# Kernel tuning notes

Hardware: AMD Instinct MI355X
Metric: run time of the kernel (lower is better)

## Reference

```python
import math
import jax, jax.numpy as jnp
import numpy as np

B, IMG, CIN = 32, 32, 4
PATCH, HIDDEN, DEPTH, HEADS, MLP = 2, 768, 12, 12, 3072
FREQ, NUM_CLASSES = 256, 1000
GRID = IMG // PATCH
N = GRID * GRID
OUT = PATCH * PATCH * CIN


def _pos_embed(dim, length):
    # faithful port of get_2d_sincos_pos_embed
    g = int(math.sqrt(length))
    grid = np.stack(np.meshgrid(np.arange(g, dtype=np.float32),
                                np.arange(g, dtype=np.float32), indexing='ij')).reshape(2, -1)
    def emb1d(d, pos):
        omega = 1.0 / 10000.0 ** (np.arange(d // 2, dtype=np.float32) / (d / 2.0))
        out = np.einsum('m,d->md', pos, omega)
        return np.concatenate([np.sin(out), np.cos(out)], axis=1)
    pe = np.concatenate([emb1d(dim // 2, grid[0]), emb1d(dim // 2, grid[1])], axis=1)
    return jnp.asarray(pe[None], dtype=jnp.float32)  # [1, N, dim]


def _ln(x):
    # LayerNorm(elementwise_affine=False), eps=1e-5, biased variance
    m = jnp.mean(x, axis=-1, keepdims=True)
    v = jnp.var(x, axis=-1, keepdims=True)
    return (x - m) * jax.lax.rsqrt(v + 1e-5)


def setup_inputs() -> dict:
    key = jax.random.key(0)
    ks = jax.random.split(key, 20)
    w = lambda k, shape: jax.random.normal(k, shape, jnp.float32) * 0.02
    z = lambda *shape: jnp.zeros(shape, jnp.float32)
    return {
        'x': jax.random.normal(ks[0], (B, IMG, IMG, CIN), jnp.float32),
        't': jax.random.uniform(ks[1], (B,), jnp.float32) * 1000.0,
        'y': jax.random.randint(ks[2], (B,), 0, NUM_CLASSES + 1),
        'patch_w': w(ks[3], (PATCH * PATCH * CIN, HIDDEN)), 'patch_b': z(HIDDEN),
        't_w1': w(ks[4], (FREQ, HIDDEN)), 't_b1': z(HIDDEN),
        't_w2': w(ks[5], (HIDDEN, HIDDEN)), 't_b2': z(HIDDEN),
        'label_emb': w(ks[6], (NUM_CLASSES + 1, HIDDEN)),
        'ada_w': w(ks[7], (DEPTH, HIDDEN, 6 * HIDDEN)), 'ada_b': z(DEPTH, 6 * HIDDEN),
        'q_w': w(ks[8], (DEPTH, HIDDEN, HIDDEN)), 'q_b': z(DEPTH, HIDDEN),
        'k_w': w(ks[9], (DEPTH, HIDDEN, HIDDEN)), 'k_b': z(DEPTH, HIDDEN),
        'v_w': w(ks[10], (DEPTH, HIDDEN, HIDDEN)), 'v_b': z(DEPTH, HIDDEN),
        'o_w': w(ks[11], (DEPTH, HIDDEN, HIDDEN)), 'o_b': z(DEPTH, HIDDEN),
        'fc1_w': w(ks[12], (DEPTH, HIDDEN, MLP)), 'fc1_b': z(DEPTH, MLP),
        'fc2_w': w(ks[13], (DEPTH, MLP, HIDDEN)), 'fc2_b': z(DEPTH, HIDDEN),
        'fin_ada_w': w(ks[14], (HIDDEN, 2 * HIDDEN)), 'fin_ada_b': z(2 * HIDDEN),
        'fin_w': w(ks[15], (HIDDEN, OUT)), 'fin_b': z(OUT),
    }


def reference(x, t, y, patch_w, patch_b, t_w1, t_b1, t_w2, t_b2, label_emb,
              ada_w, ada_b, q_w, q_b, k_w, k_b, v_w, v_b, o_w, o_b,
              fc1_w, fc1_b, fc2_w, fc2_b, fin_ada_w, fin_ada_b, fin_w, fin_b):
    Bx = x.shape[0]
    dh = HIDDEN // HEADS
    # patch embed (conv k=p, stride=p == per-patch linear)
    patches = x.reshape(Bx, GRID, PATCH, GRID, PATCH, CIN)
    patches = patches.transpose(0, 1, 3, 2, 4, 5).reshape(Bx, N, PATCH * PATCH * CIN)
    h = patches @ patch_w + patch_b + _pos_embed(HIDDEN, N)
    # timestep embedding: [cos, sin] order
    half = FREQ // 2
    freqs = jnp.exp(-math.log(10000.0) * jnp.arange(half, dtype=jnp.float32) / half)
    args = t.astype(jnp.float32)[:, None] * freqs[None]
    temb = jnp.concatenate([jnp.cos(args), jnp.sin(args)], axis=-1)
    temb = jax.nn.silu(temb @ t_w1 + t_b1) @ t_w2 + t_b2
    c_act = jax.nn.silu(temb + label_emb[y])  # silu applied inside each block on c

    def block(hx, p):
        aw, ab, qw, qb, kw, kb, vw, vb, ow, ob, f1w, f1b, f2w, f2b = p
        ada = c_act @ aw + ab
        sh_m, sc_m, g_m, sh_p, sc_p, g_p = jnp.split(ada, 6, axis=-1)
        xn = _ln(hx) * (1.0 + sc_m[:, None]) + sh_m[:, None]
        q = ((xn @ qw + qb).reshape(Bx, N, HEADS, dh)) / math.sqrt(3.0)
        k = (xn @ kw + kb).reshape(Bx, N, HEADS, dh)
        v = (xn @ vw + vb).reshape(Bx, N, HEADS, dh)
        attn = jax.nn.softmax(jnp.einsum('bqhc,bkhc->bhqk', q, k).astype(jnp.float32), axis=-1)
        yv = jnp.einsum('bhqk,bkhc->bqhc', attn, v).reshape(Bx, N, HIDDEN)
        hx = hx + g_m[:, None] * (yv @ ow + ob)
        xn2 = _ln(hx) * (1.0 + sc_p[:, None]) + sh_p[:, None]
        mlp = jax.nn.gelu(xn2 @ f1w + f1b, approximate=False) @ f2w + f2b
        hx = hx + g_p[:, None] * mlp
        return hx, None

    h, _ = jax.lax.scan(block, h, (ada_w, ada_b, q_w, q_b, k_w, k_b, v_w, v_b,
                                   o_w, o_b, fc1_w, fc1_b, fc2_w, fc2_b))
    # final layer
    fada = c_act @ fin_ada_w + fin_ada_b
    sh, sc = jnp.split(fada, 2, axis=-1)
    out = (_ln(h) * (1.0 + sc[:, None]) + sh[:, None]) @ fin_w + fin_b
    return out  # [B, N, patch*patch*out_channels]
```

## Files before the change

### kernel.cpp

```cpp
#include <hip/hip_runtime.h>
#include <hip/hip_bf16.h>


typedef short  s16x8 __attribute__((ext_vector_type(8)));
typedef float  f32x4 __attribute__((ext_vector_type(4)));

__device__ __forceinline__ float bf2f(unsigned short u) {
    union { unsigned int i; float f; } v; v.i = ((unsigned int)u) << 16; return v.f;
}
__device__ __forceinline__ unsigned short f2bf(float f) {
    union { float f; unsigned int i; } v; v.f = f;
    unsigned int r = (v.i + 0x7FFFu + ((v.i >> 16) & 1u)) >> 16;
    return (unsigned short)r;
}
__device__ __forceinline__ float silu(float v) { return v / (1.f + __expf(-v)); }

__device__ __forceinline__ void gload16(const void* gptr, void* lptr) {
    __builtin_amdgcn_global_load_lds(
        (const __attribute__((address_space(1))) unsigned int*)gptr,
        (__attribute__((address_space(3))) unsigned int*)lptr,
        16, 0, 0);
}

#define ROWS 8192
#define HID  768
#define MLPD 3072
#define ADA_LD 4608

__global__ __launch_bounds__(256) void ada_init(const float* __restrict__ ada_b,
                                                const float* __restrict__ fada_b,
                                                const float* __restrict__ t_b1,
                                                const float* __restrict__ t_b2,
                                                const float* __restrict__ lemb,
                                                const int* __restrict__ y,
                                                float* __restrict__ ada_all,
                                                float* __restrict__ fada,
                                                float* __restrict__ z1,
                                                float* __restrict__ z2)
{
    const int bid = blockIdx.x, tid = threadIdx.x;
    if (bid >= 222) {
        const int col = (bid - 222) * 256 + tid;
        const float b1v = t_b1[col], b2v = t_b2[col];
        for (int r = 0; r < 32; ++r) {
            z1[(size_t)r * HID + col] = b1v;
            z2[(size_t)r * HID + col] = b2v + lemb[(size_t)y[r] * HID + col];
        }
        return;
    }
    const float* Bv; float* Out; int ldw, colb;
    if (bid < 216) {
        const int l = bid / 18; colb = (bid % 18) * 256;
        Bv = ada_b + (size_t)l * ADA_LD; Out = ada_all + (size_t)l * 32 * ADA_LD; ldw = ADA_LD;
    } else {
        colb = (bid - 216) * 256;
        Bv = fada_b; Out = fada; ldw = 1536;
    }
    const int col = colb + tid;
    const float bb = Bv[col];
    #pragma unroll
    for (int r = 0; r < 32; ++r) Out[(size_t)r * ldw + col] = bb;
}

__global__ __launch_bounds__(256) void temb1_k(const float* __restrict__ t,
                                               const float* __restrict__ w1,
                                               float* __restrict__ z1)
{
    __shared__ float tin[128];
    const int b = blockIdx.x, cc = blockIdx.y, kc = blockIdx.z, tid = threadIdx.x;
    const int k0 = kc * 128;
    if (tid < 128) {
        const int k = k0 + tid, j = k & 127;
        const float fr = __expf((float)j * (-9.210340371976184f / 128.f));
        const float a = t[b] * fr;
        tin[tid] = (k < 128) ? cosf(a) : sinf(a);
    }
    __syncthreads();
    const int col = cc * 256 + tid;
    float acc = 0.f;
    #pragma unroll 8
    for (int kk = 0; kk < 128; ++kk) acc += tin[kk] * w1[(size_t)(k0 + kk) * HID + col];
    atomicAdd(&z1[(size_t)b * HID + col], acc);
}

__global__ __launch_bounds__(256) void temb2_k(const float* __restrict__ z1,
                                               const float* __restrict__ w2,
                                               float* __restrict__ z2)
{
    __shared__ float tin[192];
    const int b = blockIdx.x, cc = blockIdx.y, kc = blockIdx.z, tid = threadIdx.x;
    const int k0 = kc * 192;
    if (tid < 192) tin[tid] = silu(z1[(size_t)b * HID + k0 + tid]);
    __syncthreads();
    const int col = cc * 256 + tid;
    float acc = 0.f;
    #pragma unroll 8
    for (int kk = 0; kk < 192; ++kk) acc += tin[kk] * w2[(size_t)(k0 + kk) * HID + col];
    atomicAdd(&z2[(size_t)b * HID + col], acc);
}

__global__ __launch_bounds__(256) void csilu_k(const float* __restrict__ z2,
                                               unsigned short* __restrict__ cact_bf)
{
    const int base = (blockIdx.x * 256 + threadIdx.x) * 8;
    #pragma unroll
    for (int i = 0; i < 8; ++i)
        cact_bf[base + i] = f2bf(silu(z2[base + i]));
}

__global__ __launch_bounds__(256) void ada_gemm2(const float* __restrict__ z2,
                                                 const float* __restrict__ ada_w,
                                                 const float* __restrict__ fada_w,
                                                 float* __restrict__ ada_all,
                                                 float* __restrict__ fada)
{
    const int bx = blockIdx.x, kc = blockIdx.y, tid = threadIdx.x;
    const float* W; float* Out; int ldw, colb;
    if (bx < 216) {
        const int l = bx / 18; colb = (bx % 18) * 256;
        W = ada_w + (size_t)l * HID * ADA_LD; Out = ada_all + (size_t)l * 32 * ADA_LD; ldw = ADA_LD;
    } else {
        colb = (bx - 216) * 256;
        W = fada_w; Out = fada; ldw = 1536;
    }
    const int col = colb + tid;
    const int k0 = kc * 96;
    __shared__ float cs_[32][96];
    for (int i = tid; i < 32 * 96; i += 256)
        cs_[i / 96][i % 96] = silu(z2[(size_t)(i / 96) * HID + k0 + (i % 96)]);
    __syncthreads();
    float acc[32];
    #pragma unroll
    for (int r = 0; r < 32; ++r) acc[r] = 0.f;
    #pragma unroll 2
    for (int kk = 0; kk < 96; kk += 4) {
        const float w0 = W[(size_t)(k0 + kk) * ldw + col];
        const float w1 = W[(size_t)(k0 + kk + 1) * ldw + col];
        const float w2 = W[(size_t)(k0 + kk + 2) * ldw + col];
        const float w3 = W[(size_t)(k0 + kk + 3) * ldw + col];
        #pragma unroll
        for (int r = 0; r < 32; ++r) {
            const float4 cv = *(const float4*)&cs_[r][kk];
            acc[r] += cv.x * w0 + cv.y * w1 + cv.z * w2 + cv.w * w3;
        }
    }
    #pragma unroll
    for (int r = 0; r < 32; ++r) atomicAdd(&Out[(size_t)r * ldw + col], acc[r]);
}

__global__ __launch_bounds__(256) void ada_mfma(const unsigned short* __restrict__ cact_bf,
                                                const unsigned short* __restrict__ adaT,
                                                const unsigned short* __restrict__ fadaT,
                                                const float* __restrict__ ada_b,
                                                const float* __restrict__ fada_b,
                                                float* __restrict__ ada_all,
                                                float* __restrict__ fada)
{
    __shared__ unsigned short sB[2][8192];
    const int bx = blockIdx.x, tid = threadIdx.x;
    const unsigned short* Bt; const float* bias; float* Out; int ldw, colb;
    if (bx < 216) {
        const int l = bx / 18; colb = (bx % 18) * 256;
        Bt = adaT + (size_t)l * ADA_LD * HID;
        bias = ada_b + (size_t)l * ADA_LD;
        Out = ada_all + (size_t)l * 32 * ADA_LD; ldw = ADA_LD;
    } else {
        colb = (bx - 216) * 256;
        Bt = fadaT; bias = fada_b; Out = fada; ldw = 1536;
    }
    const int lane = tid & 63, w = tid >> 6;
    const int lm = lane & 15, lg = lane >> 4;
    auto stageB = [&](int buf, int kt) {
        #pragma unroll
        for (int g = 0; g < 4; ++g) {
            const int gi = g * 256 + tid;
            const int col = gi >> 2, k8 = (gi & 3) * 8;
            gload16(Bt + (size_t)(colb + col) * HID + kt * 32 + k8,
                    &sB[buf][0] + (size_t)gi * 8);
        }
    };
    f32x4 acc[2][4];
    #pragma unroll
    for (int i = 0; i < 2; ++i)
        #pragma unroll
        for (int j = 0; j < 4; ++j) acc[i][j] = (f32x4){0.f, 0.f, 0.f, 0.f};
    stageB(0, 0);
    __syncthreads();
    int cur = 0;
    for (int kt = 0; kt < 24; ++kt) {
        if (kt + 1 < 24) stageB(cur ^ 1, kt + 1);
        s16x8 af[2], bfr[4];
        #pragma unroll
        for (int mi = 0; mi < 2; ++mi)
            af[mi] = *(const s16x8*)(cact_bf + (size_t)(mi * 16 + lm) * HID + kt * 32 + lg * 8);
        #pragma unroll
        for (int nj = 0; nj < 4; ++nj)
            bfr[nj] = *(const s16x8*)&sB[cur][(w * 64 + nj * 16 + lm) * 32 + lg * 8];
        #pragma unroll
        for (int mi = 0; mi < 2; ++mi)
            #pragma unroll
            for (int nj = 0; nj < 4; ++nj)
                acc[mi][nj] = __builtin_amdgcn_mfma_f32_16x16x32_bf16(af[mi], bfr[nj], acc[mi][nj], 0, 0, 0);
        __syncthreads();
        cur ^= 1;
    }
    #pragma unroll
    for (int mi = 0; mi < 2; ++mi) {
        const int row = mi * 16 + (lg << 2);
        #pragma unroll
        for (int nj = 0; nj < 4; ++nj) {
            const int col = colb + w * 64 + nj * 16 + lm;
            const float bb = bias[col];
            #pragma unroll
            for (int r = 0; r < 4; ++r)
                Out[(size_t)(row + r) * ldw + col] = acc[mi][nj][r] + bb;
        }
    }
}

__global__ __launch_bounds__(256) void patch_embed(const float* __restrict__ x,
                                                   const float* __restrict__ pw,
                                                   const float* __restrict__ pb,
                                                   float* __restrict__ h)
{
    const int row = blockIdx.x;
    const int b = row >> 8, n = row & 255;
    const int gi = n >> 4, gj = n & 15;
    const int tid = threadIdx.x;
    __shared__ float pv[16];
    if (tid < 16) {
        const int pr = tid >> 3, pc = (tid >> 2) & 1, ci = tid & 3;
        pv[tid] = x[((size_t)(b * 32 + gi * 2 + pr) * 32 + (gj * 2 + pc)) * 4 + ci];
    }
    __syncthreads();
    #pragma unroll
    for (int cc = 0; cc < 3; ++cc) {
        const int col = cc * 256 + tid;
        float acc = pb[col];
        #pragma unroll
        for (int i = 0; i < 16; ++i) acc += pv[i] * pw[(size_t)i * HID + col];
        const int d4 = (col < 384) ? col : col - 384;
        const int pos = (col < 384) ? gi : gj;
        const float kf = (float)(d4 < 192 ? d4 : d4 - 192);
        const float om = __expf(kf * (-9.210340371976184f / 192.f));
        const float a = (float)pos * om;
        acc += (d4 < 192) ? sinf(a) : cosf(a);
        h[(size_t)row * HID + col] = acc;
    }
}

__global__ __launch_bounds__(256) void convert_weights(
    const float* __restrict__ q_w, const float* __restrict__ k_w,
    const float* __restrict__ v_w, const float* __restrict__ o_w,
    const float* __restrict__ fc1_w, const float* __restrict__ fc2_w,
    const float* __restrict__ q_b, const float* __restrict__ k_b,
    const float* __restrict__ v_b,
    unsigned short* __restrict__ wbase, size_t slot_stride,
    float* __restrict__ cbias, int first_layer)
{
    const int bid = blockIdx.x;
    const int l = first_layer + bid / 6913;
    const int t = bid % 6913;
    unsigned short* dst = wbase + (size_t)(bid / 6913) * slot_stride;
    const int tid = threadIdx.x;
    if (t == 6912) {
        float* cb = cbias + (size_t)l * 2304;
        for (int i = tid; i < 2304; i += 256) {
            float v;
            if (i < 768)       v = q_b[(size_t)l * 768 + i];
            else if (i < 1536) v = k_b[(size_t)l * 768 + i - 768];
            else               v = v_b[(size_t)l * 768 + i - 1536];
            cb[i] = v;
        }
        return;
    }
    const float* src; int srcN; unsigned short* d; int dLd; int tr, tc;
    if (t < 2304) {
        const int mat = t / 576, tt = t % 576; tr = tt / 24; tc = tt % 24;
        srcN = 768; dLd = 768;
        if (mat == 0)      { src = q_w + (size_t)l * 589824; d = dst; }
        else if (mat == 1) { src = k_w + (size_t)l * 589824; d = dst + 589824; }
        else if (mat == 2) { src = v_w + (size_t)l * 589824; d = dst + 1179648; }
        else               { src = o_w + (size_t)l * 589824; d = dst + 1769472; }
    } else if (t < 4608) {
        const int tt = t - 2304; tr = tt / 96; tc = tt % 96;
        src = fc1_w + (size_t)l * 2359296; srcN = 3072; dLd = 768; d = dst + 2359296;
    } else {
        const int tt = t - 4608; tr = tt / 24; tc = tt % 24;
        src = fc2_w + (size_t)l * 2359296; srcN = 768; dLd = 3072; d = dst + 4718592;
    }
    __shared__ float lt[32][33];
    const int tx = tid & 31, ty = tid >> 5;
    const int r0 = tr * 32, c0 = tc * 32;
    #pragma unroll
    for (int i = 0; i < 4; ++i)
        lt[ty + i * 8][tx] = src[(size_t)(r0 + ty + i * 8) * srcN + c0 + tx];
    __syncthreads();
    const int q = tid & 15;
    const int cw = tid >> 4;
    #pragma unroll
    for (int i = 0; i < 2; ++i) {
        const int cc = cw + i * 16;
        const unsigned int pk = (unsigned int)f2bf(lt[2 * q][cc])
                              | ((unsigned int)f2bf(lt[2 * q + 1][cc]) << 16);
        *(unsigned int*)&d[(size_t)(c0 + cc) * dLd + r0 + 2 * q] = pk;
    }
}

__global__ __launch_bounds__(256) void convert_ada(
    const float* __restrict__ ada_w, const float* __restrict__ fada_w,
    unsigned short* __restrict__ adaT, unsigned short* __restrict__ fadaT)
{
    const int bid = blockIdx.x, tid = threadIdx.x;
    const float* src; unsigned short* d; int srcN, tr, tc;
    if (bid < 41472) {
        const int l = bid / 3456, tt = bid % 3456;
        tr = tt / 144; tc = tt % 144;
        src = ada_w + (size_t)l * HID * ADA_LD; srcN = ADA_LD;
        d = adaT + (size_t)l * ADA_LD * HID;
    } else {
        const int tt = bid - 41472;
        tr = tt / 48; tc = tt % 48;
        src = fada_w; srcN = 1536; d = fadaT;
    }
    __shared__ float lt[32][33];
    const int tx = tid & 31, ty = tid >> 5;
    const int r0 = tr * 32, c0 = tc * 32;
    #pragma unroll
    for (int i = 0; i < 4; ++i)
        lt[ty + i * 8][tx] = src[(size_t)(r0 + ty + i * 8) * srcN + c0 + tx];
    __syncthreads();
    const int q = tid & 15;
    const int cw = tid >> 4;
    #pragma unroll
    for (int i = 0; i < 2; ++i) {
        const int cc = cw + i * 16;
        const unsigned int pk = (unsigned int)f2bf(lt[2 * q][cc])
                              | ((unsigned int)f2bf(lt[2 * q + 1][cc]) << 16);
        *(unsigned int*)&d[(size_t)(c0 + cc) * HID + r0 + 2 * q] = pk;
    }
}

__global__ __launch_bounds__(192) void ln_mod(const float* __restrict__ hbuf,
                                              const float* __restrict__ mod,
                                              int sh_off, int sc_off, int mld,
                                              unsigned short* __restrict__ xout)
{
    const int row = blockIdx.x, tid = threadIdx.x;
    const float4 xv = *(const float4*)&hbuf[(size_t)row * HID + tid * 4];
    float s = (xv.x + xv.y) + (xv.z + xv.w);
    float ss = (xv.x * xv.x + xv.y * xv.y) + (xv.z * xv.z + xv.w * xv.w);
    #pragma unroll
    for (int d = 1; d < 64; d <<= 1) { s += __shfl_xor(s, d); ss += __shfl_xor(ss, d); }
    __shared__ float sb[3], ssb[3];
    if ((tid & 63) == 0) { sb[tid >> 6] = s; ssb[tid >> 6] = ss; }
    __syncthreads();
    s = sb[0] + sb[1] + sb[2];
    ss = ssb[0] + ssb[1] + ssb[2];
    const float mean = s * (1.f / 768.f);
    const float var = ss * (1.f / 768.f) - mean * mean;
    const float rs = rsqrtf(var + 1e-5f);
    const int b = row >> 8;
    const float* mrow = mod + (size_t)b * mld;
    const float4 sc = *(const float4*)&mrow[sc_off + tid * 4];
    const float4 sh = *(const float4*)&mrow[sh_off + tid * 4];
    ushort4 o;
    o.x = f2bf((xv.x - mean) * rs * (1.f + sc.x) + sh.x);
    o.y = f2bf((xv.y - mean) * rs * (1.f + sc.y) + sh.y);
    o.z = f2bf((xv.z - mean) * rs * (1.f + sc.z) + sh.z);
    o.w = f2bf((xv.w - mean) * rs * (1.f + sc.w) + sh.w);
    *(ushort4*)&xout[(size_t)row * HID + tid * 4] = o;
}

template<int EPI, int BN>
__global__ __launch_bounds__(256) void gemm_bt(const unsigned short* __restrict__ A,
                                               const unsigned short* __restrict__ Bt,
                                               const float* __restrict__ bias,
                                               void* __restrict__ outp,
                                               const float* __restrict__ gate,
                                               int K, int ldo)
{
    constexpr int BELEMS = BN * 32;
    constexpr int NJ = BN / 32;
    __shared__ unsigned short sAB[2][4096 + BELEMS];
    const int tid = threadIdx.x;
    const int lane = tid & 63;
    const int w = tid >> 6;
    const int wm = w >> 1, wn = w & 1;
    const int nwg = gridDim.x * gridDim.y;
    int bidl = blockIdx.y * gridDim.x + blockIdx.x;
    bidl = (bidl & 7) * (nwg >> 3) + (bidl >> 3);
    const int bx = bidl % gridDim.x, by = bidl / gridDim.x;
    const int rowbase = by << 7;
    const int colbase = bx * BN;
    const size_t a0 = (size_t)(rowbase +      (tid >> 2)) * K + (tid & 3) * 8;
    const size_t a1 = (size_t)(rowbase + 64 + (tid >> 2)) * K + (tid & 3) * 8;
    const size_t b0 = (size_t)(colbase +      (tid >> 2)) * K + (tid & 3) * 8;
    size_t b1 = 0;
    if constexpr (BN == 128)
        b1 = (size_t)(colbase + 64 + (tid >> 2)) * K + (tid & 3) * 8;
    const int ldsw = w * 512;
    f32x4 acc[4][NJ];
    #pragma unroll
    for (int i = 0; i < 4; ++i)
        #pragma unroll
        for (int j = 0; j < NJ; ++j) acc[i][j] = (f32x4){0.f, 0.f, 0.f, 0.f};
    const int nk = K >> 5;
    const int lm = lane & 15, lg = lane >> 4;
    {
        unsigned short* base = &sAB[0][0];
        gload16(A + a0,  base + ldsw);
        gload16(A + a1,  base + 2048 + ldsw);
        gload16(Bt + b0, base + 4096 + ldsw);
        if constexpr (BN == 128) gload16(Bt + b1, base + 6144 + ldsw);
    }
    __syncthreads();
    int cur = 0;
    for (int kt = 0; kt < nk; ++kt) {
        if (kt + 1 < nk) {
            const int k0 = (kt + 1) << 5;
            unsigned short* base = &sAB[cur ^ 1][0];
            gload16(A + a0 + k0,  base + ldsw);
            gload16(A + a1 + k0,  base + 2048 + ldsw);
            gload16(Bt + b0 + k0, base + 4096 + ldsw);
            if constexpr (BN == 128) gload16(Bt + b1 + k0, base + 6144 + ldsw);
        }
        const unsigned short* sAc = &sAB[cur][0];
        const unsigned short* sBc = &sAB[cur][4096];
        s16x8 af[4], bfr[NJ];
        #pragma unroll
        for (int mi = 0; mi < 4; ++mi)
            af[mi] = *(const s16x8*)&sAc[(wm * 64 + mi * 16 + lm) * 32 + lg * 8];
        #pragma unroll
        for (int nj = 0; nj < NJ; ++nj)
            bfr[nj] = *(const s16x8*)&sBc[(wn * (16 * NJ) + nj * 16 + lm) * 32 + lg * 8];
        #pragma unroll
        for (int mi = 0; mi < 4; ++mi)
            #pragma unroll
            for (int nj = 0; nj < NJ; ++nj)
                acc[mi][nj] = __builtin_amdgcn_mfma_f32_16x16x32_bf16(af[mi], bfr[nj], acc[mi][nj], 0, 0, 0);
        __syncthreads();
        cur ^= 1;
    }
    float bv[NJ], gv[NJ];
    #pragma unroll
    for (int nj = 0; nj < NJ; ++nj) {
        const int col = colbase + wn * (16 * NJ) + nj * 16 + lm;
        bv[nj] = bias[col];
        if constexpr (EPI == 2) gv[nj] = gate[(size_t)(rowbase >> 8) * ADA_LD + col];
    }
    #pragma unroll
    for (int mi = 0; mi < 4; ++mi) {
        const int row = rowbase + wm * 64 + mi * 16 + (lg << 2);
        #pragma unroll
        for (int nj = 0; nj < NJ; ++nj) {
            const int col = colbase + wn * (16 * NJ) + nj * 16 + lm;
            #pragma unroll
            for (int r = 0; r < 4; ++r) {
                const float v = acc[mi][nj][r] + bv[nj];
                if constexpr (EPI == 0) {
                    ((unsigned short*)outp)[(size_t)(row + r) * ldo + col] = f2bf(v);
                } else if constexpr (EPI == 1) {
                    const float g = 0.5f * v * (1.f + erff(v * 0.70710678118654752f));
                    ((unsigned short*)outp)[(size_t)(row + r) * ldo + col] = f2bf(g);
                } else {
                    float* O = (float*)outp;
                    const size_t idx = (size_t)(row + r) * ldo + col;
                    O[idx] = O[idx] + gv[nj] * v;
                }
            }
        }
    }
}

__global__ __launch_bounds__(256) void attn_fused(const unsigned short* __restrict__ qkv,
                                                  unsigned short* __restrict__ yv)
{
    __shared__ unsigned short Vt[64][264];
    __shared__ unsigned short Psm[4][32 * 72];
    __shared__ float Ssc[4][32];
    const int bid = blockIdx.x;
    const int b = bid / 24, rem = bid % 24, h = rem >> 1, half = rem & 1;
    const int tid = threadIdx.x, w = tid >> 6, lane = tid & 63;
    {
        const int dhg = tid & 7, tk = tid >> 3;
        #pragma unroll
        for (int g = 0; g < 8; ++g) {
            const int tok = tk + g * 32;
            s16x8 vv = *(const s16x8*)(qkv + (size_t)(b * 256 + tok) * 2304 + 1536 + h * 64 + dhg * 8);
            #pragma unroll
            for (int j = 0; j < 8; ++j) Vt[dhg * 8 + j][tok] = (unsigned short)vv[j];
        }
    }
    __syncthreads();
    const int q0 = half * 128 + w * 32;
    const int lm = lane & 15, lg = lane >> 4;
    const unsigned short* Qb = qkv + (size_t)(b * 256 + q0) * 2304 + h * 64;
    s16x8 qf[2][2];
    #pragma unroll
    for (int ni = 0; ni < 2; ++ni)
        #pragma unroll
        for (int kk = 0; kk < 2; ++kk)
            qf[ni][kk] = *(const s16x8*)(Qb + (size_t)(ni * 16 + lm) * 2304 + kk * 32 + lg * 8);
    f32x4 o_[2][4];
    #pragma unroll
    for (int i = 0; i < 2; ++i)
        #pragma unroll
        for (int j = 0; j < 4; ++j) o_[i][j] = (f32x4){0.f, 0.f, 0.f, 0.f};
    float m_[2], l_[2];
    #pragma unroll
    for (int i = 0; i < 2; ++i) { m_[i] = -1e30f; l_[i] = 0.f; }
    const float s3 = 0.57735026918962576f;
    for (int c = 0; c < 4; ++c) {
        f32x4 st[4][2];
        #pragma unroll
        for (int i = 0; i < 4; ++i)
            #pragma unroll
            for (int j = 0; j < 2; ++j) st[i][j] = (f32x4){0.f, 0.f, 0.f, 0.f};
        const unsigned short* Kb = qkv + (size_t)(b * 256 + c * 64) * 2304 + 768 + h * 64;
        __builtin_amdgcn_s_setprio(1);
        #pragma unroll
        for (int kk = 0; kk < 2; ++kk)
            #pragma unroll
            for (int mi = 0; mi < 4; ++mi) {
                const s16x8 kf = *(const s16x8*)(Kb + (size_t)(mi * 16 + lm) * 2304 + kk * 32 + lg * 8);
                #pragma unroll
                for (int ni = 0; ni < 2; ++ni)
                    st[mi][ni] = __builtin_amdgcn_mfma_f32_16x16x32_bf16(kf, qf[ni][kk], st[mi][ni], 0, 0, 0);
            }
        __builtin_amdgcn_s_setprio(0);
        #pragma unroll
        for (int ni = 0; ni < 2; ++ni) {
            float cm = -1e30f;
            #pragma unroll
            for (int mi = 0; mi < 4; ++mi)
                #pragma unroll
                for (int r = 0; r < 4; ++r) cm = fmaxf(cm, st[mi][ni][r]);
            cm = fmaxf(cm, __shfl_xor(cm, 16));
            cm = fmaxf(cm, __shfl_xor(cm, 32));
            cm *= s3;
            const float mn = fmaxf(m_[ni], cm);
            const float corr = __expf(m_[ni] - mn);
            float cs = 0.f;
            #pragma unroll
            for (int mi = 0; mi < 4; ++mi) {
                float p0 = __expf(st[mi][ni][0] * s3 - mn);
                float p1 = __expf(st[mi][ni][1] * s3 - mn);
                float p2 = __expf(st[mi][ni][2] * s3 - mn);
                float p3 = __expf(st[mi][ni][3] * s3 - mn);
                cs += (p0 + p1) + (p2 + p3);
                uint2 pk;
                pk.x = (unsigned int)f2bf(p0) | ((unsigned int)f2bf(p1) << 16);
                pk.y = (unsigned int)f2bf(p2) | ((unsigned int)f2bf(p3) << 16);
                *(uint2*)&Psm[w][(ni * 16 + lm) * 72 + mi * 16 + lg * 4] = pk;
            }
            cs += __shfl_xor(cs, 16);
            cs += __shfl_xor(cs, 32);
            l_[ni] = l_[ni] * corr + cs;
            m_[ni] = mn;
            if (lane < 16) Ssc[w][ni * 16 + lane] = corr;
        }
        asm volatile("" ::: "memory");
        #pragma unroll
        for (int qi = 0; qi < 2; ++qi) {
            float fr[4];
            #pragma unroll
            for (int r = 0; r < 4; ++r) fr[r] = Ssc[w][qi * 16 + lg * 4 + r];
            #pragma unroll
            for (int di = 0; di < 4; ++di)
                #pragma unroll
                for (int r = 0; r < 4; ++r) o_[qi][di][r] *= fr[r];
        }
        __builtin_amdgcn_s_setprio(1);
        #pragma unroll
        for (int kk = 0; kk < 2; ++kk)
            #pragma unroll
            for (int qi = 0; qi < 2; ++qi) {
                const s16x8 pa = *(const s16x8*)&Psm[w][(qi * 16 + lm) * 72 + kk * 32 + lg * 8];
                #pragma unroll
                for (int di = 0; di < 4; ++di) {
                    const s16x8 vb = *(const s16x8*)&Vt[di * 16 + lm][c * 64 + kk * 32 + lg * 8];
                    o_[qi][di] = __builtin_amdgcn_mfma_f32_16x16x32_bf16(pa, vb, o_[qi][di], 0, 0, 0);
                }
            }
        __builtin_amdgcn_s_setprio(0);
    }
    asm volatile("" ::: "memory");
    if (lane < 16) {
        #pragma unroll
        for (int ni = 0; ni < 2; ++ni) Ssc[w][ni * 16 + lane] = 1.f / l_[ni];
    }
    asm volatile("" ::: "memory");
    #pragma unroll
    for (int qi = 0; qi < 2; ++qi) {
        float fr[4];
        #pragma unroll
        for (int r = 0; r < 4; ++r) fr[r] = Ssc[w][qi * 16 + lg * 4 + r];
        #pragma unroll
        for (int di = 0; di < 4; ++di)
            #pragma unroll
            for (int r = 0; r < 4; ++r) {
                const float val = o_[qi][di][r] * fr[r];
                yv[(size_t)(b * 256 + q0 + qi * 16 + lg * 4 + r) * HID + h * 64 + di * 16 + lm] = f2bf(val);
            }
    }
}

__global__ __launch_bounds__(256) void fin_gemm(const unsigned short* __restrict__ xn,
                                                const float* __restrict__ w,
                                                const float* __restrict__ bias,
                                                float* __restrict__ out)
{
    __shared__ unsigned short xs[16 * 768];
    const int rb = blockIdx.x * 16, tid = threadIdx.x;
    #pragma unroll
    for (int i = 0; i < 6; ++i) {
        const int v = tid + i * 256;
        const int row = v / 96, koff = (v % 96) * 8;
        *(s16x8*)&xs[v * 8] = *(const s16x8*)(xn + (size_t)(rb + row) * HID + koff);
    }
    __syncthreads();
    const int r = tid >> 4, o = tid & 15;
    float acc = bias[o];
    #pragma unroll 8
    for (int k = 0; k < 768; ++k) acc += bf2f(xs[r * 768 + k]) * w[(size_t)k * 16 + o];
    out[(size_t)(rb + r) * 16 + o] = acc;
}

extern "C" void kernel_launch(void* const* d_in, const int* in_sizes, int n_in,
                              void* d_out, int out_size, void* d_ws, size_t ws_size,
                              hipStream_t stream)
{
    const float* x        = (const float*)d_in[0];
    const float* t        = (const float*)d_in[1];
    const int*   y        = (const int*)d_in[2];
    const float* patch_w  = (const float*)d_in[3];
    const float* patch_b  = (const float*)d_in[4];
    const float* t_w1     = (const float*)d_in[5];
    const float* t_b1     = (const float*)d_in[6];
    const float* t_w2     = (const float*)d_in[7];
    const float* t_b2     = (const float*)d_in[8];
    const float* label_e  = (const float*)d_in[9];
    const float* ada_w    = (const float*)d_in[10];
    const float* ada_b    = (const float*)d_in[11];
    const float* q_w      = (const float*)d_in[12];
    const float* q_b      = (const float*)d_in[13];
    const float* k_w      = (const float*)d_in[14];
    const float* k_b      = (const float*)d_in[15];
    const float* v_w      = (const float*)d_in[16];
    const float* v_b      = (const float*)d_in[17];
    const float* o_w      = (const float*)d_in[18];
    const float* o_b      = (const float*)d_in[19];
    const float* fc1_w    = (const float*)d_in[20];
    const float* fc1_b    = (const float*)d_in[21];
    const float* fc2_w    = (const float*)d_in[22];
    const float* fc2_b    = (const float*)d_in[23];
    const float* fada_w   = (const float*)d_in[24];
    const float* fada_b   = (const float*)d_in[25];
    const float* fin_w    = (const float*)d_in[26];
    const float* fin_b    = (const float*)d_in[27];

    char* ws = (char*)d_ws;
    size_t off = 0;
    auto alloc = [&](size_t bytes) { size_t o = off; off = (off + bytes + 255) & ~(size_t)255; return o; };
    const size_t OFF_H     = alloc((size_t)ROWS * HID * 4);
    const size_t OFF_XN    = alloc((size_t)ROWS * HID * 2);
    const size_t OFF_QKV   = alloc((size_t)ROWS * 2304 * 2);
    const size_t OFF_YV    = alloc((size_t)ROWS * HID * 2);
    const size_t OFF_MLP   = alloc((size_t)ROWS * MLPD * 2);
    const size_t OFF_ADA   = alloc((size_t)12 * 32 * ADA_LD * 4);
    const size_t OFF_FADA  = alloc((size_t)32 * 1536 * 4);
    const size_t OFF_Z2    = alloc((size_t)32 * HID * 4);
    const size_t OFF_Z1    = alloc((size_t)32 * HID * 4);
    const size_t OFF_CB    = alloc((size_t)12 * 2304 * 4);
    const size_t OFF_CBF   = alloc((size_t)32 * HID * 2);
    const size_t OFF_ADAT  = alloc((size_t)12 * ADA_LD * HID * 2);
    const size_t OFF_FADAT = alloc((size_t)1536 * HID * 2);
    const size_t OFF_W     = off;
    const size_t WSLOT_ELEMS = 7077888;
    const bool big = (ws_size >= OFF_W + (size_t)12 * WSLOT_ELEMS * 2);

    float*          h     = (float*)(ws + OFF_H);
    unsigned short* xn    = (unsigned short*)(ws + OFF_XN);
    unsigned short* qkv   = (unsigned short*)(ws + OFF_QKV);
    unsigned short* yv    = (unsigned short*)(ws + OFF_YV);
    unsigned short* mlp   = (unsigned short*)(ws + OFF_MLP);
    float*          adaA  = (float*)(ws + OFF_ADA);
    float*          fada  = (float*)(ws + OFF_FADA);
    float*          z2    = (float*)(ws + OFF_Z2);
    float*          z1    = (float*)(ws + OFF_Z1);
    float*          cbias = (float*)(ws + OFF_CB);
    unsigned short* cactb = (unsigned short*)(ws + OFF_CBF);
    unsigned short* adaT  = (unsigned short*)(ws + OFF_ADAT);
    unsigned short* fadaT = (unsigned short*)(ws + OFF_FADAT);
    unsigned short* wsW   = (unsigned short*)(ws + OFF_W);

    ada_init<<<225, 256, 0, stream>>>(ada_b, fada_b, t_b1, t_b2, label_e, y,
                                      adaA, fada, z1, z2);
    temb1_k<<<dim3(32, 3, 2), 256, 0, stream>>>(t, t_w1, z1);
    temb2_k<<<dim3(32, 3, 4), 256, 0, stream>>>(z1, t_w2, z2);
    if (big) {
        convert_ada<<<42624, 256, 0, stream>>>(ada_w, fada_w, adaT, fadaT);
        csilu_k<<<12, 256, 0, stream>>>(z2, cactb);
        ada_mfma<<<222, 256, 0, stream>>>(cactb, adaT, fadaT, ada_b, fada_b, adaA, fada);
        convert_weights<<<6913 * 12, 256, 0, stream>>>(q_w, k_w, v_w, o_w, fc1_w, fc2_w,
                                                       q_b, k_b, v_b, wsW, WSLOT_ELEMS, cbias, 0);
    } else {
        ada_gemm2<<<dim3(222, 8), 256, 0, stream>>>(z2, ada_w, fada_w, adaA, fada);
    }
    patch_embed<<<8192, 256, 0, stream>>>(x, patch_w, patch_b, h);

    for (int l = 0; l < 12; ++l) {
        unsigned short* wslot = wsW + (big ? (size_t)l * WSLOT_ELEMS : 0);
        if (!big) {
            convert_weights<<<6913, 256, 0, stream>>>(q_w, k_w, v_w, o_w, fc1_w, fc2_w,
                                                      q_b, k_b, v_b, wslot, 0, cbias, l);
        }
        unsigned short* qkvT = wslot;
        unsigned short* oT   = wslot + 1769472;
        unsigned short* f1T  = wslot + 2359296;
        unsigned short* f2T  = wslot + 4718592;
        float* ada_l  = adaA + (size_t)l * 32 * ADA_LD;
        float* cb_l   = cbias + (size_t)l * 2304;

        ln_mod<<<8192, 192, 0, stream>>>(h, ada_l, 0, 768, ADA_LD, xn);
        gemm_bt<0, 128><<<dim3(18, 64), 256, 0, stream>>>(xn, qkvT, cb_l, qkv, nullptr, 768, 2304);
        attn_fused<<<768, 256, 0, stream>>>(qkv, yv);
        gemm_bt<2, 64><<<dim3(12, 64), 256, 0, stream>>>(yv, oT, o_b + (size_t)l * 768, h,
                                                         ada_l + 1536, 768, 768);
        ln_mod<<<8192, 192, 0, stream>>>(h, ada_l, 2304, 3072, ADA_LD, xn);
        gemm_bt<1, 128><<<dim3(24, 64), 256, 0, stream>>>(xn, f1T, fc1_b + (size_t)l * 3072, mlp,
                                                          nullptr, 768, 3072);
        gemm_bt<2, 64><<<dim3(12, 64), 256, 0, stream>>>(mlp, f2T, fc2_b + (size_t)l * 768, h,
                                                         ada_l + 3840, 3072, 768);
    }

    ln_mod<<<8192, 192, 0, stream>>>(h, fada, 0, 768, 1536, xn);
    fin_gemm<<<512, 256, 0, stream>>>(xn, fin_w, fin_b, (float*)d_out);
}
```

Before: 3.404 ms.

## Fuse ada weight transpose-convert into ada GEMM and batch LN rows

Removes the separate convert_ada pass, which transposed and converted all adaLN weights to bf16 through a workspace buffer. ada_mfma now reads the fp32 weights directly and converts and packs them into shared memory while staging. The ada_init launch is trimmed to the three timestep blocks when the MFMA path runs. ln_mod now handles four rows per block with a quarter of the launches, adding extra block barriers, and the inline staging loses the asynchronous global-to-LDS loads.

```diff
diff --git a/kernel.cpp b/kernel.cpp
--- a/kernel.cpp
+++ b/kernel.cpp
@@ -36,9 +36,10 @@
                                                 float* __restrict__ ada_all,
                                                 float* __restrict__ fada,
                                                 float* __restrict__ z1,
-                                                float* __restrict__ z2)
-{
-    const int bid = blockIdx.x, tid = threadIdx.x;
+                                                float* __restrict__ z2,
+                                                int bid0)
+{
+    const int bid = blockIdx.x + bid0, tid = threadIdx.x;
     if (bid >= 222) {
         const int col = (bid - 222) * 256 + tid;
         const float b1v = t_b1[col], b2v = t_b2[col];
@@ -149,8 +150,8 @@
 }
 
 __global__ __launch_bounds__(256) void ada_mfma(const unsigned short* __restrict__ cact_bf,
-                                                const unsigned short* __restrict__ adaT,
-                                                const unsigned short* __restrict__ fadaT,
+                                                const float* __restrict__ ada_w,
+                                                const float* __restrict__ fada_w,
                                                 const float* __restrict__ ada_b,
                                                 const float* __restrict__ fada_b,
                                                 float* __restrict__ ada_all,
@@ -158,25 +159,35 @@
 {
     __shared__ unsigned short sB[2][8192];
     const int bx = blockIdx.x, tid = threadIdx.x;
-    const unsigned short* Bt; const float* bias; float* Out; int ldw, colb;
+    const float* W; const float* bias; float* Out; int ldw, colb;
     if (bx < 216) {
         const int l = bx / 18; colb = (bx % 18) * 256;
-        Bt = adaT + (size_t)l * ADA_LD * HID;
+        W = ada_w + (size_t)l * HID * ADA_LD;
         bias = ada_b + (size_t)l * ADA_LD;
         Out = ada_all + (size_t)l * 32 * ADA_LD; ldw = ADA_LD;
     } else {
         colb = (bx - 216) * 256;
-        Bt = fadaT; bias = fada_b; Out = fada; ldw = 1536;
+        W = fada_w; bias = fada_b; Out = fada; ldw = 1536;
     }
     const int lane = tid & 63, w = tid >> 6;
     const int lm = lane & 15, lg = lane >> 4;
+    const int kp = tid & 15, cg = tid >> 4;
     auto stageB = [&](int buf, int kt) {
-        #pragma unroll
-        for (int g = 0; g < 4; ++g) {
-            const int gi = g * 256 + tid;
-            const int col = gi >> 2, k8 = (gi & 3) * 8;
-            gload16(Bt + (size_t)(colb + col) * HID + kt * 32 + k8,
-                    &sB[buf][0] + (size_t)gi * 8);
+        const float* r0 = W + (size_t)(kt * 32 + 2 * kp) * ldw + colb + cg * 16;
+        const float* r1 = r0 + ldw;
+        unsigned int* dst = (unsigned int*)&sB[buf][0];
+        #pragma unroll
+        for (int c4 = 0; c4 < 4; ++c4) {
+            const float4 a = *(const float4*)(r0 + c4 * 4);
+            const float4 b = *(const float4*)(r1 + c4 * 4);
+            const float av[4] = {a.x, a.y, a.z, a.w};
+            const float bv4[4] = {b.x, b.y, b.z, b.w};
+            #pragma unroll
+            for (int c = 0; c < 4; ++c) {
+                const int col = cg * 16 + c4 * 4 + c;
+                dst[col * 16 + kp] = (unsigned int)f2bf(av[c])
+                                   | ((unsigned int)f2bf(bv4[c]) << 16);
+            }
         }
     };
     f32x4 acc[2][4];
@@ -307,69 +318,40 @@
     }
 }
 
-__global__ __launch_bounds__(256) void convert_ada(
-    const float* __restrict__ ada_w, const float* __restrict__ fada_w,
-    unsigned short* __restrict__ adaT, unsigned short* __restrict__ fadaT)
-{
-    const int bid = blockIdx.x, tid = threadIdx.x;
-    const float* src; unsigned short* d; int srcN, tr, tc;
-    if (bid < 41472) {
-        const int l = bid / 3456, tt = bid % 3456;
-        tr = tt / 144; tc = tt % 144;
-        src = ada_w + (size_t)l * HID * ADA_LD; srcN = ADA_LD;
-        d = adaT + (size_t)l * ADA_LD * HID;
-    } else {
-        const int tt = bid - 41472;
-        tr = tt / 48; tc = tt % 48;
-        src = fada_w; srcN = 1536; d = fadaT;
-    }
-    __shared__ float lt[32][33];
-    const int tx = tid & 31, ty = tid >> 5;
-    const int r0 = tr * 32, c0 = tc * 32;
-    #pragma unroll
-    for (int i = 0; i < 4; ++i)
-        lt[ty + i * 8][tx] = src[(size_t)(r0 + ty + i * 8) * srcN + c0 + tx];
-    __syncthreads();
-    const int q = tid & 15;
-    const int cw = tid >> 4;
-    #pragma unroll
-    for (int i = 0; i < 2; ++i) {
-        const int cc = cw + i * 16;
-        const unsigned int pk = (unsigned int)f2bf(lt[2 * q][cc])
-                              | ((unsigned int)f2bf(lt[2 * q + 1][cc]) << 16);
-        *(unsigned int*)&d[(size_t)(c0 + cc) * HID + r0 + 2 * q] = pk;
-    }
-}
-
 __global__ __launch_bounds__(192) void ln_mod(const float* __restrict__ hbuf,
                                               const float* __restrict__ mod,
                                               int sh_off, int sc_off, int mld,
                                               unsigned short* __restrict__ xout)
 {
-    const int row = blockIdx.x, tid = threadIdx.x;
-    const float4 xv = *(const float4*)&hbuf[(size_t)row * HID + tid * 4];
-    float s = (xv.x + xv.y) + (xv.z + xv.w);
-    float ss = (xv.x * xv.x + xv.y * xv.y) + (xv.z * xv.z + xv.w * xv.w);
-    #pragma unroll
-    for (int d = 1; d < 64; d <<= 1) { s += __shfl_xor(s, d); ss += __shfl_xor(ss, d); }
+    const int tid = threadIdx.x;
     __shared__ float sb[3], ssb[3];
-    if ((tid & 63) == 0) { sb[tid >> 6] = s; ssb[tid >> 6] = ss; }
-    __syncthreads();
-    s = sb[0] + sb[1] + sb[2];
-    ss = ssb[0] + ssb[1] + ssb[2];
-    const float mean = s * (1.f / 768.f);
-    const float var = ss * (1.f / 768.f) - mean * mean;
-    const float rs = rsqrtf(var + 1e-5f);
-    const int b = row >> 8;
-    const float* mrow = mod + (size_t)b * mld;
-    const float4 sc = *(const float4*)&mrow[sc_off + tid * 4];
-    const float4 sh = *(const float4*)&mrow[sh_off + tid * 4];
-    ushort4 o;
-    o.x = f2bf((xv.x - mean) * rs * (1.f + sc.x) + sh.x);
-    o.y = f2bf((xv.y - mean) * rs * (1.f + sc.y) + sh.y);
-    o.z = f2bf((xv.z - mean) * rs * (1.f + sc.z) + sh.z);
-    o.w = f2bf((xv.w - mean) * rs * (1.f + sc.w) + sh.w);
-    *(ushort4*)&xout[(size_t)row * HID + tid * 4] = o;
+    #pragma unroll
+    for (int rr = 0; rr < 4; ++rr) {
+        const int row = blockIdx.x * 4 + rr;
+        const float4 xv = *(const float4*)&hbuf[(size_t)row * HID + tid * 4];
+        float s = (xv.x + xv.y) + (xv.z + xv.w);
+        float ss = (xv.x * xv.x + xv.y * xv.y) + (xv.z * xv.z + xv.w * xv.w);
+        #pragma unroll
+        for (int d = 1; d < 64; d <<= 1) { s += __shfl_xor(s, d); ss += __shfl_xor(ss, d); }
+        if ((tid & 63) == 0) { sb[tid >> 6] = s; ssb[tid >> 6] = ss; }
+        __syncthreads();
+        s = sb[0] + sb[1] + sb[2];
+        ss = ssb[0] + ssb[1] + ssb[2];
+        const float mean = s * (1.f / 768.f);
+        const float var = ss * (1.f / 768.f) - mean * mean;
+        const float rs = rsqrtf(var + 1e-5f);
+        const int b = row >> 8;
+        const float* mrow = mod + (size_t)b * mld;
+        const float4 sc = *(const float4*)&mrow[sc_off + tid * 4];
+        const float4 sh = *(const float4*)&mrow[sh_off + tid * 4];
+        ushort4 o;
+        o.x = f2bf((xv.x - mean) * rs * (1.f + sc.x) + sh.x);
+        o.y = f2bf((xv.y - mean) * rs * (1.f + sc.y) + sh.y);
+        o.z = f2bf((xv.z - mean) * rs * (1.f + sc.z) + sh.z);
+        o.w = f2bf((xv.w - mean) * rs * (1.f + sc.w) + sh.w);
+        *(ushort4*)&xout[(size_t)row * HID + tid * 4] = o;
+        __syncthreads();
+    }
 }
 
 template<int EPI, int BN>
@@ -674,8 +656,6 @@
     const size_t OFF_Z1    = alloc((size_t)32 * HID * 4);
     const size_t OFF_CB    = alloc((size_t)12 * 2304 * 4);
     const size_t OFF_CBF   = alloc((size_t)32 * HID * 2);
-    const size_t OFF_ADAT  = alloc((size_t)12 * ADA_LD * HID * 2);
-    const size_t OFF_FADAT = alloc((size_t)1536 * HID * 2);
     const size_t OFF_W     = off;
     const size_t WSLOT_ELEMS = 7077888;
     const bool big = (ws_size >= OFF_W + (size_t)12 * WSLOT_ELEMS * 2);
@@ -691,18 +671,20 @@
     float*          z1    = (float*)(ws + OFF_Z1);
     float*          cbias = (float*)(ws + OFF_CB);
     unsigned short* cactb = (unsigned short*)(ws + OFF_CBF);
-    unsigned short* adaT  = (unsigned short*)(ws + OFF_ADAT);
-    unsigned short* fadaT = (unsigned short*)(ws + OFF_FADAT);
     unsigned short* wsW   = (unsigned short*)(ws + OFF_W);
 
-    ada_init<<<225, 256, 0, stream>>>(ada_b, fada_b, t_b1, t_b2, label_e, y,
-                                      adaA, fada, z1, z2);
+    if (big) {
+        ada_init<<<3, 256, 0, stream>>>(ada_b, fada_b, t_b1, t_b2, label_e, y,
+                                        adaA, fada, z1, z2, 222);
+    } else {
+        ada_init<<<225, 256, 0, stream>>>(ada_b, fada_b, t_b1, t_b2, label_e, y,
+                                          adaA, fada, z1, z2, 0);
+    }
     temb1_k<<<dim3(32, 3, 2), 256, 0, stream>>>(t, t_w1, z1);
     temb2_k<<<dim3(32, 3, 4), 256, 0, stream>>>(z1, t_w2, z2);
     if (big) {
-        convert_ada<<<42624, 256, 0, stream>>>(ada_w, fada_w, adaT, fadaT);
         csilu_k<<<12, 256, 0, stream>>>(z2, cactb);
-        ada_mfma<<<222, 256, 0, stream>>>(cactb, adaT, fadaT, ada_b, fada_b, adaA, fada);
+        ada_mfma<<<222, 256, 0, stream>>>(cactb, ada_w, fada_w, ada_b, fada_b, adaA, fada);
         convert_weights<<<6913 * 12, 256, 0, stream>>>(q_w, k_w, v_w, o_w, fc1_w, fc2_w,
                                                        q_b, k_b, v_b, wsW, WSLOT_ELEMS, cbias, 0);
     } else {
@@ -723,18 +705,18 @@
         float* ada_l  = adaA + (size_t)l * 32 * ADA_LD;
         float* cb_l   = cbias + (size_t)l * 2304;
 
-        ln_mod<<<8192, 192, 0, stream>>>(h, ada_l, 0, 768, ADA_LD, xn);
+        ln_mod<<<2048, 192, 0, stream>>>(h, ada_l, 0, 768, ADA_LD, xn);
         gemm_bt<0, 128><<<dim3(18, 64), 256, 0, stream>>>(xn, qkvT, cb_l, qkv, nullptr, 768, 2304);
         attn_fused<<<768, 256, 0, stream>>>(qkv, yv);
         gemm_bt<2, 64><<<dim3(12, 64), 256, 0, stream>>>(yv, oT, o_b + (size_t)l * 768, h,
                                                          ada_l + 1536, 768, 768);
-        ln_mod<<<8192, 192, 0, stream>>>(h, ada_l, 2304, 3072, ADA_LD, xn);
+        ln_mod<<<2048, 192, 0, stream>>>(h, ada_l, 2304, 3072, ADA_LD, xn);
         gemm_bt<1, 128><<<dim3(24, 64), 256, 0, stream>>>(xn, f1T, fc1_b + (size_t)l * 3072, mlp,
                                                           nullptr, 768, 3072);
         gemm_bt<2, 64><<<dim3(12, 64), 256, 0, stream>>>(mlp, f2T, fc2_b + (size_t)l * 768, h,
                                                          ada_l + 3840, 3072, 768);
     }
 
-    ln_mod<<<8192, 192, 0, stream>>>(h, fada, 0, 768, 1536, xn);
+    ln_mod<<<2048, 192, 0, stream>>>(h, fada, 0, 768, 1536, xn);
     fin_gemm<<<512, 256, 0, stream>>>(xn, fin_w, fin_b, (float*)d_out);
 }
```

Result: faster. 3.331 ms (-2.1%).
